# Performance work log

Hardware: AMD Instinct MI355X
Metric: run time of the kernel (lower is better)

The kernel has to match this reference:

```python
import jax, jax.numpy as jnp
import numpy as np

LN_EPS = 1e-5


def layer_norm(x, gamma, beta):
    mu = jnp.mean(x, axis=-1, keepdims=True)
    var = jnp.mean(jnp.square(x - mu), axis=-1, keepdims=True)
    return (x - mu) * jax.lax.rsqrt(var + LN_EPS) * gamma + beta


def setup_inputs() -> dict:
    key = jax.random.key(0)
    ks = jax.random.split(key, 4)
    b, t, d, h, r = 4, 2048, 1024, 4096, 32
    x = jax.random.normal(ks[0], (b, t, d), dtype=jnp.float32)
    L = jax.random.normal(ks[1], (d, r), dtype=jnp.float32) * (1.0 / np.sqrt(d))
    W1 = jax.random.normal(ks[2], (d, h), dtype=jnp.float32) * (1.0 / np.sqrt(d))
    W2 = jax.random.normal(ks[3], (h, d), dtype=jnp.float32) * (1.0 / np.sqrt(h))
    return {
        "x": x, "L": L,
        "W1": W1, "b1": jnp.zeros((h,), jnp.float32),
        "W2": W2, "b2": jnp.zeros((d,), jnp.float32),
        "gamma1": jnp.ones((d,), jnp.float32), "beta1": jnp.zeros((d,), jnp.float32),
        "gamma2": jnp.ones((d,), jnp.float32), "beta2": jnp.zeros((d,), jnp.float32),
    }


def reference(x, L, W1, b1, W2, b2, gamma1, beta1, gamma2, beta2):
    d = x.shape[-1]
    # --- GeodesicAttention on norm1(x) ---
    hn = layer_norm(x, gamma1, beta1)  # (b,t,d)
    g = jnp.eye(d, dtype=x.dtype) + L @ L.T  # PSD metric G = I + L L^T, (d,d)
    # dist_sq[b,i,j] = (x_i - x_j)^T G (x_i - x_j)
    #               = q_i + q_j - 2 x_i^T G x_j   (quadratic expansion; avoids (b,t,t,d) diff tensor)
    xg = jnp.einsum('btd,de->bte', hn, g)          # G x, (b,t,d)
    q = jnp.einsum('btd,btd->bt', xg, hn)          # diag quadratic form, (b,t)
    cross = jnp.einsum('bid,bjd->bij', xg, hn)     # x_i^T G x_j, (b,t,t)
    dist_sq = q[:, :, None] + q[:, None, :] - 2.0 * cross
    attn = jax.nn.softmax(-dist_sq, axis=-1)       # (b,t,t)
    x = x + jnp.einsum('bij,bjd->bid', attn, hn)
    # --- MLP on norm2(x) ---
    hm = layer_norm(x, gamma2, beta2)
    hid = jax.nn.gelu(hm @ W1 + b1, approximate=False)
    x = x + hid @ W2 + b2
    return x
```

## Files before the change

kernel.cpp:

```cpp
#include <hip/hip_runtime.h>
#include <cstdint>

typedef float f32x4 __attribute__((ext_vector_type(4)));
typedef __bf16 bf16x8 __attribute__((ext_vector_type(8)));

#define AS1 __attribute__((address_space(1)))
#define AS3 __attribute__((address_space(3)))

__device__ __forceinline__ void gld_lds16(const void* g, void* l) {
    __builtin_amdgcn_global_load_lds((const AS1 void*)g, (AS3 void*)l, 16, 0, 0);
}

__device__ __forceinline__ unsigned short f2bf(float f) {
    unsigned u = __builtin_bit_cast(unsigned, f);
    u = u + 0x7fffu + ((u >> 16) & 1u);
    return (unsigned short)(u >> 16);
}
__device__ __forceinline__ float bf2f(unsigned short h) {
    unsigned u = ((unsigned)h) << 16;
    return __builtin_bit_cast(float, u);
}

__device__ __forceinline__ void bar() {
    asm volatile("" ::: "memory");
    __builtin_amdgcn_s_barrier();
    asm volatile("" ::: "memory");
}

template<int BN, int MODE>
__global__ __launch_bounds__(512, 2) void gemm_nt2(
    const unsigned short* __restrict__ A, long lda, long sAb,
    const unsigned short* __restrict__ B, long ldb, long sBb,
    void* C, long ldc, long sCb,
    const float* add, long ldadd, long sAddb,
    const float* __restrict__ bias, int K)
{
    constexpr int NR  = BN / 64;
    constexpr int BUF = 16384 + BN * 64;
    __shared__ char sm[4 * BUF];
    const int tid = threadIdx.x, lane = tid & 63, wid = tid >> 6;
    const int wr = wid >> 2, wc = wid & 3;

    const long zb = blockIdx.z;
    const int nwg  = gridDim.x * gridDim.y;
    const int orig = blockIdx.y * gridDim.x + blockIdx.x;
    const int q8 = nwg >> 3, r8 = nwg & 7;
    const int xcd = orig & 7;
    const int wg  = (xcd < r8 ? xcd * (q8 + 1) : r8 * (q8 + 1) + (xcd - r8) * q8) + (orig >> 3);
    const int bx = wg % gridDim.x, by = wg / gridDim.x;

    const char* Ab = (const char*)(A + zb * sAb + (long)by * 256 * lda);
    const char* Bb = (const char*)(B + zb * sBb + (long)bx * BN * ldb);
    const long ldaB = lda * 2, ldbB = ldb * 2;
    const int  grow = tid >> 2;
    const long gcol = (long)(tid & 3) * 16;

    auto stage = [&](int kt, int bi) {
        const char* As = Ab + (long)kt * 64 + gcol;
        const char* Bs = Bb + (long)kt * 64 + gcol;
        char* d = sm + bi * BUF + wid * 1024;
#pragma unroll
        for (int i = 0; i < 2; ++i)
            gld_lds16(As + (long)(i * 128 + grow) * ldaB, d + i * 8192);
#pragma unroll
        for (int i = 0; i < BN / 128; ++i)
            gld_lds16(Bs + (long)(i * 128 + grow) * ldbB, d + 16384 + i * 8192);
    };

    f32x4 acc[8][NR] = {};
    const int NT = K / 32;
    stage(0, 0);
    if (NT > 1) stage(1, 1);
    if (NT > 2) stage(2, 2);

    for (int t = 0; t < NT; ++t) {
        const int rem = NT - t;
        if (rem > 3) {
            stage(t + 3, (t + 3) & 3);
            if constexpr (BN == 256) asm volatile("s_waitcnt vmcnt(12)" ::: "memory");
            else                     asm volatile("s_waitcnt vmcnt(9)"  ::: "memory");
        } else if (rem == 3) {
            if constexpr (BN == 256) asm volatile("s_waitcnt vmcnt(8)" ::: "memory");
            else                     asm volatile("s_waitcnt vmcnt(6)" ::: "memory");
        } else if (rem == 2) {
            if constexpr (BN == 256) asm volatile("s_waitcnt vmcnt(4)" ::: "memory");
            else                     asm volatile("s_waitcnt vmcnt(3)" ::: "memory");
        } else {
            asm volatile("s_waitcnt vmcnt(0)" ::: "memory");
        }
        bar();

        const char* bufA = sm + (t & 3) * BUF;
        const char* bufB = bufA + 16384;
        bf16x8 af[8], bfr[NR];
#pragma unroll
        for (int m = 0; m < 8; ++m)
            af[m] = *(const bf16x8*)(bufA + (wr * 128 + m * 16 + (lane & 15)) * 64 + (lane >> 4) * 16);
#pragma unroll
        for (int n = 0; n < NR; ++n)
            bfr[n] = *(const bf16x8*)(bufB + (wc * 16 * NR + n * 16 + (lane & 15)) * 64 + (lane >> 4) * 16);
        __builtin_amdgcn_s_setprio(1);
#pragma unroll
        for (int m = 0; m < 8; ++m)
#pragma unroll
            for (int n = 0; n < NR; ++n)
                acc[m][n] = __builtin_amdgcn_mfma_f32_16x16x32_bf16(af[m], bfr[n], acc[m][n], 0, 0, 0);
        __builtin_amdgcn_s_setprio(0);
        asm volatile("s_waitcnt lgkmcnt(0)" ::: "memory");
        __builtin_amdgcn_sched_barrier(0);
        bar();
    }

    const long row0 = (long)by * 256 + wr * 128 + (lane >> 4) * 4;
    const long col0 = (long)bx * BN + wc * 16 * NR + (lane & 15);
#pragma unroll
    for (int m = 0; m < 8; ++m)
#pragma unroll
        for (int n = 0; n < NR; ++n)
#pragma unroll
            for (int j = 0; j < 4; ++j) {
                const long r = row0 + m * 16 + j;
                const long c = col0 + n * 16;
                const float v = acc[m][n][j];
                if (MODE == 0) {
                    ((float*)C)[zb * sCb + r * ldc + c] = v;
                } else if (MODE == 1) {
                    ((float*)C)[zb * sCb + r * ldc + c] = v + add[zb * sAddb + r * ldadd + c];
                } else if (MODE == 2) {
                    float tt = v + bias[c];
                    float gl = 0.5f * tt * (1.0f + erff(tt * 0.70710678118654752f));
                    ((unsigned short*)C)[zb * sCb + r * ldc + c] = f2bf(gl);
                } else {
                    ((float*)C)[zb * sCb + r * ldc + c] = v + bias[c] + add[zb * sAddb + r * ldadd + c];
                }
            }
}

__global__ __launch_bounds__(256) void ln_kernel(
    const float* __restrict__ x, const float* __restrict__ gamma, const float* __restrict__ beta,
    unsigned short* __restrict__ out, int ldout, float* qout, int pad)
{
    const int tid = threadIdx.x;
    const long row = blockIdx.x;
    float4 v = ((const float4*)(x + row * 1024))[tid];
    float s = v.x + v.y + v.z + v.w;
    float s2 = v.x * v.x + v.y * v.y + v.z * v.z + v.w * v.w;
#pragma unroll
    for (int off = 32; off; off >>= 1) {
        s  += __shfl_down(s, off);
        s2 += __shfl_down(s2, off);
    }
    __shared__ float red[12];
    const int lane = tid & 63, wid = tid >> 6;
    if (lane == 0) { red[wid] = s; red[4 + wid] = s2; }
    __syncthreads();
    s  = red[0] + red[1] + red[2] + red[3];
    s2 = red[4] + red[5] + red[6] + red[7];
    const float mu = s * (1.0f / 1024.0f);
    const float var = s2 * (1.0f / 1024.0f) - mu * mu;
    const float rs = rsqrtf(var + 1e-5f);
    const float4 g = ((const float4*)gamma)[tid];
    const float4 b = ((const float4*)beta)[tid];
    unsigned short o0 = f2bf((v.x - mu) * rs * g.x + b.x);
    unsigned short o1 = f2bf((v.y - mu) * rs * g.y + b.y);
    unsigned short o2 = f2bf((v.z - mu) * rs * g.z + b.z);
    unsigned short o3 = f2bf((v.w - mu) * rs * g.w + b.w);
    ushort4 ov; ov.x = o0; ov.y = o1; ov.z = o2; ov.w = o3;
    ((ushort4*)(out + row * (long)ldout))[tid] = ov;
    if (pad && tid < 32) out[row * (long)ldout + 1056 + tid] = 0;
    if (qout) {
        float y0 = bf2f(o0), y1 = bf2f(o1), y2 = bf2f(o2), y3 = bf2f(o3);
        float sq = y0 * y0 + y1 * y1 + y2 * y2 + y3 * y3;
#pragma unroll
        for (int off = 32; off; off >>= 1) sq += __shfl_down(sq, off);
        if (lane == 0) red[8 + wid] = sq;
        __syncthreads();
        if (tid == 0) qout[row] = red[8] + red[9] + red[10] + red[11];
    }
}

__global__ __launch_bounds__(256) void u_kernel(
    unsigned short* __restrict__ z, const float* __restrict__ L, float* __restrict__ q)
{
    const int tid = threadIdx.x;
    const long row = blockIdx.x;
    __shared__ float hn[1024];
    __shared__ float part[8][32];
    ushort4 uv = ((const ushort4*)(z + row * 1088))[tid];
    hn[tid * 4 + 0] = bf2f(uv.x);
    hn[tid * 4 + 1] = bf2f(uv.y);
    hn[tid * 4 + 2] = bf2f(uv.z);
    hn[tid * 4 + 3] = bf2f(uv.w);
    __syncthreads();
    const int j = tid & 31, grp = tid >> 5;
    float acc = 0.f;
    const float* Lp = L + j;
#pragma unroll 4
    for (int d = grp * 128; d < grp * 128 + 128; ++d)
        acc += hn[d] * Lp[(long)d * 32];
    part[grp][j] = acc;
    __syncthreads();
    if (tid < 32) {
        float u = 0.f;
#pragma unroll
        for (int g2 = 0; g2 < 8; ++g2) u += part[g2][tid];
        unsigned short ub = f2bf(u);
        z[row * 1088 + 1024 + tid] = ub;
        float uf = bf2f(ub);
        part[0][tid] = uf * uf;
    }
    __syncthreads();
    if (tid == 0) {
        float sq = 0.f;
#pragma unroll
        for (int t2 = 0; t2 < 32; ++t2) sq += part[0][t2];
        q[row] += sq;
    }
}

__global__ __launch_bounds__(256) void softmax_kernel(
    float* S, const float* qb)
{
    const int tid = threadIdx.x;
    const long i = blockIdx.x, bl = blockIdx.y;
    float* Sr = S + (bl * 2048 + i) * 2048;
    const float* qr = qb + bl * 2048;
    float l[8];
    float mx = -1e30f;
#pragma unroll
    for (int c2 = 0; c2 < 8; ++c2) {
        const int jj = tid + c2 * 256;
        l[c2] = 2.0f * Sr[jj] - qr[jj];
        mx = fmaxf(mx, l[c2]);
    }
#pragma unroll
    for (int off = 32; off; off >>= 1) mx = fmaxf(mx, __shfl_xor(mx, off));
    __shared__ float red[8];
    const int lane = tid & 63, wid = tid >> 6;
    if (lane == 0) red[wid] = mx;
    __syncthreads();
    mx = fmaxf(fmaxf(red[0], red[1]), fmaxf(red[2], red[3]));
    float sum = 0.f;
#pragma unroll
    for (int c2 = 0; c2 < 8; ++c2) { l[c2] = __expf(l[c2] - mx); sum += l[c2]; }
#pragma unroll
    for (int off = 32; off; off >>= 1) sum += __shfl_xor(sum, off);
    if (lane == 0) red[4 + wid] = sum;
    __syncthreads();
    sum = red[4] + red[5] + red[6] + red[7];
    const float inv = 1.0f / sum;
    unsigned short* Pr = (unsigned short*)S + (bl * 2048 + i) * 4096;
#pragma unroll
    for (int c2 = 0; c2 < 8; ++c2)
        Pr[tid + c2 * 256] = f2bf(l[c2] * inv);
}

__global__ __launch_bounds__(256) void transpose_v_kernel(
    const unsigned short* __restrict__ z, unsigned short* __restrict__ Vt, long sVtb)
{
    __shared__ unsigned short t[32][33];
    const int tid = threadIdx.x;
    const int tx = tid & 31, ty = tid >> 5;
    const long b = blockIdx.z;
    const long k0 = (long)blockIdx.x * 32, n0 = (long)blockIdx.y * 32;
#pragma unroll
    for (int r = 0; r < 32; r += 8)
        t[r + ty][tx] = z[(b * 2048 + k0 + r + ty) * 1088 + n0 + tx];
    __syncthreads();
#pragma unroll
    for (int r = 0; r < 32; r += 8)
        Vt[b * sVtb + (n0 + r + ty) * 2048 + k0 + tx] = t[tx][r + ty];
}

__global__ __launch_bounds__(256) void cast_transpose_kernel(
    const float* __restrict__ W, unsigned short* __restrict__ Wt, int rows, int cols)
{
    __shared__ float t[32][33];
    const int tid = threadIdx.x;
    const int tx = tid & 31, ty = tid >> 5;
    const long r0 = (long)blockIdx.y * 32, c0 = (long)blockIdx.x * 32;
#pragma unroll
    for (int r = 0; r < 32; r += 8)
        t[r + ty][tx] = W[(r0 + r + ty) * (long)cols + c0 + tx];
    __syncthreads();
#pragma unroll
    for (int r = 0; r < 32; r += 8)
        Wt[(c0 + r + ty) * (long)rows + r0 + tx] = f2bf(t[tx][r + ty]);
}

extern "C" void kernel_launch(void* const* d_in, const int* in_sizes, int n_in,
                              void* d_out, int out_size, void* d_ws, size_t ws_size,
                              hipStream_t stream)
{
    const float* x   = (const float*)d_in[0];
    const float* L   = (const float*)d_in[1];
    const float* W1  = (const float*)d_in[2];
    const float* b1  = (const float*)d_in[3];
    const float* W2  = (const float*)d_in[4];
    const float* b2  = (const float*)d_in[5];
    const float* g1  = (const float*)d_in[6];
    const float* be1 = (const float*)d_in[7];
    const float* g2  = (const float*)d_in[8];
    const float* be2 = (const float*)d_in[9];
    float* out = (float*)d_out;
    unsigned short* z = (unsigned short*)d_out;

    char* wsp = (char*)d_ws;
    float* q = (float*)wsp;
    char* pool = wsp + 32768;
    unsigned short* Vt   = (unsigned short*)pool;
    float*          Smat = (float*)(pool + 16777216);
    unsigned short* W1t = (unsigned short*)pool;
    unsigned short* W2t = (unsigned short*)(pool + 8388608);
    unsigned short* hm  = (unsigned short*)(pool + 16777216);
    unsigned short* hid = (unsigned short*)(pool + 33554432);
    const bool fullMLP = ws_size >= (size_t)32768 + 100663296 + 65536;

    ln_kernel<<<8192, 256, 0, stream>>>(x, g1, be1, z, 1088, q, 1);
    u_kernel<<<8192, 256, 0, stream>>>(z, L, q);

    transpose_v_kernel<<<dim3(64, 32, 4), 256, 0, stream>>>(z, Vt, (long)1024 * 2048);
    gemm_nt2<256, 0><<<dim3(8, 8, 4), 512, 0, stream>>>(
        z, 1088, (long)2048 * 1088,
        z, 1088, (long)2048 * 1088,
        Smat, 2048, (long)2048 * 2048,
        nullptr, 0, 0, nullptr, 1088);
    softmax_kernel<<<dim3(2048, 4), 256, 0, stream>>>(Smat, q);
    gemm_nt2<128, 1><<<dim3(8, 8, 4), 512, 0, stream>>>(
        (const unsigned short*)Smat, 4096, (long)2048 * 4096,
        Vt, 2048, (long)1024 * 2048,
        out, 1024, (long)2048 * 1024,
        x, 1024, (long)2048 * 1024,
        nullptr, 2048);

    cast_transpose_kernel<<<dim3(128, 32), 256, 0, stream>>>(W1, W1t, 1024, 4096);
    cast_transpose_kernel<<<dim3(32, 128), 256, 0, stream>>>(W2, W2t, 4096, 1024);
    ln_kernel<<<8192, 256, 0, stream>>>(out, g2, be2, hm, 1024, nullptr, 0);
    if (fullMLP) {
        gemm_nt2<256, 2><<<dim3(16, 32, 1), 512, 0, stream>>>(
            hm, 1024, 0, W1t, 1024, 0,
            hid, 4096, 0, nullptr, 0, 0, b1, 1024);
        gemm_nt2<128, 3><<<dim3(8, 32, 1), 512, 0, stream>>>(
            hid, 4096, 0, W2t, 4096, 0,
            out, 1024, 0, out, 1024, 0, b2, 4096);
    } else {
        for (int c = 0; c < 2; ++c) {
            const unsigned short* hmc = hm + (size_t)c * 4096 * 1024;
            float* oc = out + (size_t)c * 4096 * 1024;
            gemm_nt2<256, 2><<<dim3(16, 16, 1), 512, 0, stream>>>(
                hmc, 1024, 0, W1t, 1024, 0,
                hid, 4096, 0, nullptr, 0, 0, b1, 1024);
            gemm_nt2<128, 3><<<dim3(8, 16, 1), 512, 0, stream>>>(
                hid, 4096, 0, W2t, 4096, 0,
                oc, 1024, 0, oc, 1024, 0, b2, 4096);
        }
    }
}
```

Before: 392.8 us.

## Swizzle LDS tile layout and double-buffer MFMA fragments across k-steps

Each lane's 16-byte global column chunk is now chosen by an XOR swizzle, and the fragment reads use the matching swizzled offset. This spreads LDS reads across banks to cut bank conflicts. The main loop is also unrolled by two with two register sets of A/B fragments, so the next tile's LDS reads are issued before the current tile's MFMAs and overlap with them. The cost is more register pressure from the doubled fragment arrays. The loop also assumes the k-tile count is even, which holds for all call sites here.

Result: faster. 381.7 us (-2.8%).

```diff
diff --git a/kernel.cpp b/kernel.cpp
--- a/kernel.cpp
+++ b/kernel.cpp
@@ -27,8 +27,12 @@
     asm volatile("" ::: "memory");
 }
 
+#define WAITVM(n) asm volatile("s_waitcnt vmcnt(" #n ")" ::: "memory")
+#define LGKM0     asm volatile("s_waitcnt lgkmcnt(0)" ::: "memory")
+#define SCHED0    __builtin_amdgcn_sched_barrier(0)
+
 template<int BN, int MODE>
-__global__ __launch_bounds__(512, 2) void gemm_nt2(
+__global__ __launch_bounds__(512, 2) void gemm_nt3(
     const unsigned short* __restrict__ A, long lda, long sAb,
     const unsigned short* __restrict__ B, long ldb, long sBb,
     void* C, long ldc, long sCb,
@@ -53,11 +57,12 @@
     const char* Bb = (const char*)(B + zb * sBb + (long)bx * BN * ldb);
     const long ldaB = lda * 2, ldbB = ldb * 2;
     const int  grow = tid >> 2;
-    const long gcol = (long)(tid & 3) * 16;
+    const long gsw  = (long)((((lane & 3) ^ ((lane >> 2) & 3) ^ ((lane >> 4) & 1))) << 4);
+    const int  koff16 = (((lane >> 4) ^ (lane & 3) ^ ((lane >> 2) & 1)) << 4);
 
     auto stage = [&](int kt, int bi) {
-        const char* As = Ab + (long)kt * 64 + gcol;
-        const char* Bs = Bb + (long)kt * 64 + gcol;
+        const char* As = Ab + (long)kt * 64 + gsw;
+        const char* Bs = Bb + (long)kt * 64 + gsw;
         char* d = sm + bi * BUF + wid * 1024;
 #pragma unroll
         for (int i = 0; i < 2; ++i)
@@ -67,38 +72,18 @@
             gld_lds16(Bs + (long)(i * 128 + grow) * ldbB, d + 16384 + i * 8192);
     };
 
+    auto rdfrags = [&](const char* bufA, bf16x8* af, bf16x8* bfr) {
+        const char* bufB = bufA + 16384;
+#pragma unroll
+        for (int m = 0; m < 8; ++m)
+            af[m] = *(const bf16x8*)(bufA + (wr * 128 + m * 16 + (lane & 15)) * 64 + koff16);
+#pragma unroll
+        for (int n = 0; n < NR; ++n)
+            bfr[n] = *(const bf16x8*)(bufB + (wc * 16 * NR + n * 16 + (lane & 15)) * 64 + koff16);
+    };
+
     f32x4 acc[8][NR] = {};
-    const int NT = K / 32;
-    stage(0, 0);
-    if (NT > 1) stage(1, 1);
-    if (NT > 2) stage(2, 2);
-
-    for (int t = 0; t < NT; ++t) {
-        const int rem = NT - t;
-        if (rem > 3) {
-            stage(t + 3, (t + 3) & 3);
-            if constexpr (BN == 256) asm volatile("s_waitcnt vmcnt(12)" ::: "memory");
-            else                     asm volatile("s_waitcnt vmcnt(9)"  ::: "memory");
-        } else if (rem == 3) {
-            if constexpr (BN == 256) asm volatile("s_waitcnt vmcnt(8)" ::: "memory");
-            else                     asm volatile("s_waitcnt vmcnt(6)" ::: "memory");
-        } else if (rem == 2) {
-            if constexpr (BN == 256) asm volatile("s_waitcnt vmcnt(4)" ::: "memory");
-            else                     asm volatile("s_waitcnt vmcnt(3)" ::: "memory");
-        } else {
-            asm volatile("s_waitcnt vmcnt(0)" ::: "memory");
-        }
-        bar();
-
-        const char* bufA = sm + (t & 3) * BUF;
-        const char* bufB = bufA + 16384;
-        bf16x8 af[8], bfr[NR];
-#pragma unroll
-        for (int m = 0; m < 8; ++m)
-            af[m] = *(const bf16x8*)(bufA + (wr * 128 + m * 16 + (lane & 15)) * 64 + (lane >> 4) * 16);
-#pragma unroll
-        for (int n = 0; n < NR; ++n)
-            bfr[n] = *(const bf16x8*)(bufB + (wc * 16 * NR + n * 16 + (lane & 15)) * 64 + (lane >> 4) * 16);
+    auto domfma = [&](const bf16x8* af, const bf16x8* bfr) {
         __builtin_amdgcn_s_setprio(1);
 #pragma unroll
         for (int m = 0; m < 8; ++m)
@@ -106,9 +91,44 @@
             for (int n = 0; n < NR; ++n)
                 acc[m][n] = __builtin_amdgcn_mfma_f32_16x16x32_bf16(af[m], bfr[n], acc[m][n], 0, 0, 0);
         __builtin_amdgcn_s_setprio(0);
-        asm volatile("s_waitcnt lgkmcnt(0)" ::: "memory");
-        __builtin_amdgcn_sched_barrier(0);
+    };
+
+    const int NT = K / 32;
+    bf16x8 a0[8], b0[NR], a1[8], b1[NR];
+
+    stage(0, 0); stage(1, 1); stage(2, 2);
+    if constexpr (BN == 256) WAITVM(8); else WAITVM(6);
+    bar();
+    rdfrags(sm, a0, b0);
+    SCHED0;
+
+#pragma unroll 1
+    for (int t = 0; t < NT; t += 2) {
+        if (t + 3 < NT) {
+            stage(t + 3, (t + 3) & 3);
+            if constexpr (BN == 256) WAITVM(8); else WAITVM(6);
+        } else {
+            WAITVM(0);
+        }
         bar();
+        rdfrags(sm + ((t + 1) & 3) * BUF, a1, b1);
+        SCHED0;
+        domfma(a0, b0);
+        LGKM0; SCHED0;
+
+        if (t + 2 < NT) {
+            if (t + 4 < NT) {
+                stage(t + 4, (t + 4) & 3);
+                if constexpr (BN == 256) WAITVM(8); else WAITVM(6);
+            } else {
+                if constexpr (BN == 256) WAITVM(4); else WAITVM(3);
+            }
+            bar();
+            rdfrags(sm + ((t + 2) & 3) * BUF, a0, b0);
+            SCHED0;
+        }
+        domfma(a1, b1);
+        LGKM0; SCHED0;
     }
 
     const long row0 = (long)by * 256 + wr * 128 + (lane >> 4) * 4;
@@ -320,13 +340,13 @@
     u_kernel<<<8192, 256, 0, stream>>>(z, L, q);
 
     transpose_v_kernel<<<dim3(64, 32, 4), 256, 0, stream>>>(z, Vt, (long)1024 * 2048);
-    gemm_nt2<256, 0><<<dim3(8, 8, 4), 512, 0, stream>>>(
+    gemm_nt3<256, 0><<<dim3(8, 8, 4), 512, 0, stream>>>(
         z, 1088, (long)2048 * 1088,
         z, 1088, (long)2048 * 1088,
         Smat, 2048, (long)2048 * 2048,
         nullptr, 0, 0, nullptr, 1088);
     softmax_kernel<<<dim3(2048, 4), 256, 0, stream>>>(Smat, q);
-    gemm_nt2<128, 1><<<dim3(8, 8, 4), 512, 0, stream>>>(
+    gemm_nt3<128, 1><<<dim3(8, 8, 4), 512, 0, stream>>>(
         (const unsigned short*)Smat, 4096, (long)2048 * 4096,
         Vt, 2048, (long)1024 * 2048,
         out, 1024, (long)2048 * 1024,
@@ -337,20 +357,20 @@
     cast_transpose_kernel<<<dim3(32, 128), 256, 0, stream>>>(W2, W2t, 4096, 1024);
     ln_kernel<<<8192, 256, 0, stream>>>(out, g2, be2, hm, 1024, nullptr, 0);
     if (fullMLP) {
-        gemm_nt2<256, 2><<<dim3(16, 32, 1), 512, 0, stream>>>(
+        gemm_nt3<256, 2><<<dim3(16, 32, 1), 512, 0, stream>>>(
             hm, 1024, 0, W1t, 1024, 0,
             hid, 4096, 0, nullptr, 0, 0, b1, 1024);
-        gemm_nt2<128, 3><<<dim3(8, 32, 1), 512, 0, stream>>>(
+        gemm_nt3<128, 3><<<dim3(8, 32, 1), 512, 0, stream>>>(
             hid, 4096, 0, W2t, 4096, 0,
             out, 1024, 0, out, 1024, 0, b2, 4096);
     } else {
         for (int c = 0; c < 2; ++c) {
             const unsigned short* hmc = hm + (size_t)c * 4096 * 1024;
             float* oc = out + (size_t)c * 4096 * 1024;
-            gemm_nt2<256, 2><<<dim3(16, 16, 1), 512, 0, stream>>>(
+            gemm_nt3<256, 2><<<dim3(16, 16, 1), 512, 0, stream>>>(
                 hmc, 1024, 0, W1t, 1024, 0,
                 hid, 4096, 0, nullptr, 0, 0, b1, 1024);
-            gemm_nt2<128, 3><<<dim3(8, 16, 1), 512, 0, stream>>>(
+            gemm_nt3<128, 3><<<dim3(8, 16, 1), 512, 0, stream>>>(
                 hid, 4096, 0, W2t, 4096, 0,
                 oc, 1024, 0, oc, 1024, 0, b2, 4096);
         }
```

## Restructure GEMM into double-buffered 8-phase pipeline with swizzled LDS and K=64 tiles

Applied to the files above, without the earlier changes.

Replaces the 4-deep K=32 pipelined GEMM with a 2-buffer K=64 scheme. Each K tile is split into four phases that interleave half-tile global-to-LDS loads with MFMA work, and each phase has its own barrier and waitcnt. An XOR swizzle is applied to the LDS layout to avoid bank conflicts on fragment reads. The goal is finer-grained overlap of loads and compute and less LDS conflict, at the cost of more barriers and tighter vmcnt bookkeeping, which could go wrong for edge K counts. K=1088 gives NT=17, which is fine.

Result: no change. 389.5 us (-0.9%).

```diff
diff --git a/kernel.cpp b/kernel.cpp
--- a/kernel.cpp
+++ b/kernel.cpp
@@ -27,17 +27,23 @@
     asm volatile("" ::: "memory");
 }
 
+#define WAITVM(n) asm volatile("s_waitcnt vmcnt(" #n ")" ::: "memory")
+#define LGKM0     asm volatile("s_waitcnt lgkmcnt(0)" ::: "memory")
+#define SCHED0    __builtin_amdgcn_sched_barrier(0)
+
 template<int BN, int MODE>
-__global__ __launch_bounds__(512, 2) void gemm_nt2(
+__global__ __launch_bounds__(512, 2) void gemm8p(
     const unsigned short* __restrict__ A, long lda, long sAb,
     const unsigned short* __restrict__ B, long ldb, long sBb,
     void* C, long ldc, long sCb,
     const float* add, long ldadd, long sAddb,
     const float* __restrict__ bias, int K)
 {
-    constexpr int NR  = BN / 64;
-    constexpr int BUF = 16384 + BN * 64;
-    __shared__ char sm[4 * BUF];
+    constexpr int NR   = BN / 64;
+    constexpr int ABUF = 256 * 128;
+    constexpr int BBUF = BN * 128;
+    constexpr int BUF  = ABUF + BBUF;
+    __shared__ char sm[2 * BUF];
     const int tid = threadIdx.x, lane = tid & 63, wid = tid >> 6;
     const int wr = wid >> 2, wc = wid & 3;
 
@@ -52,64 +58,73 @@
     const char* Ab = (const char*)(A + zb * sAb + (long)by * 256 * lda);
     const char* Bb = (const char*)(B + zb * sBb + (long)bx * BN * ldb);
     const long ldaB = lda * 2, ldbB = ldb * 2;
-    const int  grow = tid >> 2;
-    const long gcol = (long)(tid & 3) * 16;
-
-    auto stage = [&](int kt, int bi) {
-        const char* As = Ab + (long)kt * 64 + gcol;
-        const char* Bs = Bb + (long)kt * 64 + gcol;
-        char* d = sm + bi * BUF + wid * 1024;
-#pragma unroll
-        for (int i = 0; i < 2; ++i)
-            gld_lds16(As + (long)(i * 128 + grow) * ldaB, d + i * 8192);
-#pragma unroll
-        for (int i = 0; i < BN / 128; ++i)
-            gld_lds16(Bs + (long)(i * 128 + grow) * ldbB, d + 16384 + i * 8192);
+
+    auto stageA = [&](int kt, int p, int half) {
+#pragma unroll
+        for (int i = 0; i < 2; ++i) {
+            const int r0 = half * 64 + i * 128;
+            const int r  = r0 + (tid >> 3);
+            gld_lds16(Ab + (long)r * ldaB + (long)kt * 128 + (((tid & 7) ^ (r & 7)) << 4),
+                      sm + p * BUF + r0 * 128 + wid * 1024);
+        }
     };
+    auto stageB = [&](int kt, int p, int ks) {
+#pragma unroll
+        for (int i = 0; i < BN / 128; ++i) {
+            const int r = i * 128 + (tid >> 2);
+            gld_lds16(Bb + (long)r * ldbB + (long)kt * 128 + ks * 64 + (((tid & 3) ^ ((r >> 1) & 3)) << 4),
+                      sm + p * BUF + ABUF + ks * BN * 64 + i * 8192 + wid * 1024);
+        }
+    };
 
     f32x4 acc[8][NR] = {};
-    const int NT = K / 32;
-    stage(0, 0);
-    if (NT > 1) stage(1, 1);
-    if (NT > 2) stage(2, 2);
-
+    const int NT = K / 64;
+
+#define PHASE(MH, KS, STAGE_STMT) do {                                          \
+    bf16x8 af[4]; bf16x8 bfr[NR];                                               \
+    _Pragma("unroll")                                                           \
+    for (int m = 0; m < 4; ++m) {                                               \
+        const int R = wr * 128 + ((MH) * 4 + m) * 16 + (lane & 15);             \
+        const int cc = (((KS) * 4 + (lane >> 4)) ^ (R & 7)) << 4;               \
+        af[m] = *(const bf16x8*)(bufp + R * 128 + cc);                          \
+    }                                                                           \
+    _Pragma("unroll")                                                           \
+    for (int n = 0; n < NR; ++n) {                                              \
+        const int R = wc * 16 * NR + n * 16 + (lane & 15);                      \
+        const int cc = ((lane >> 4) ^ ((R >> 1) & 3)) << 4;                     \
+        bfr[n] = *(const bf16x8*)(bufp + ABUF + (KS) * BN * 64 + R * 64 + cc);  \
+    }                                                                           \
+    STAGE_STMT;                                                                 \
+    if (t < NT - 2) { if constexpr (BN == 256) WAITVM(8); else WAITVM(6); }     \
+    else WAITVM(0);                                                             \
+    bar();                                                                      \
+    LGKM0; SCHED0;                                                              \
+    __builtin_amdgcn_s_setprio(1);                                              \
+    _Pragma("unroll")                                                           \
+    for (int m = 0; m < 4; ++m)                                                 \
+    _Pragma("unroll")                                                           \
+        for (int n = 0; n < NR; ++n)                                            \
+            acc[(MH) * 4 + m][n] = __builtin_amdgcn_mfma_f32_16x16x32_bf16(     \
+                af[m], bfr[n], acc[(MH) * 4 + m][n], 0, 0, 0);                  \
+    __builtin_amdgcn_s_setprio(0);                                              \
+    bar();                                                                      \
+} while (0)
+
+    stageA(0, 0, 0); stageA(0, 0, 1); stageB(0, 0, 0); stageB(0, 0, 1);
+    stageA(1, 1, 0); stageB(1, 1, 0); stageA(1, 1, 1); stageB(1, 1, 1);
+    if constexpr (BN == 256) WAITVM(8); else WAITVM(6);
+    bar();
+
+#pragma unroll 1
     for (int t = 0; t < NT; ++t) {
-        const int rem = NT - t;
-        if (rem > 3) {
-            stage(t + 3, (t + 3) & 3);
-            if constexpr (BN == 256) asm volatile("s_waitcnt vmcnt(12)" ::: "memory");
-            else                     asm volatile("s_waitcnt vmcnt(9)"  ::: "memory");
-        } else if (rem == 3) {
-            if constexpr (BN == 256) asm volatile("s_waitcnt vmcnt(8)" ::: "memory");
-            else                     asm volatile("s_waitcnt vmcnt(6)" ::: "memory");
-        } else if (rem == 2) {
-            if constexpr (BN == 256) asm volatile("s_waitcnt vmcnt(4)" ::: "memory");
-            else                     asm volatile("s_waitcnt vmcnt(3)" ::: "memory");
-        } else {
-            asm volatile("s_waitcnt vmcnt(0)" ::: "memory");
-        }
-        bar();
-
-        const char* bufA = sm + (t & 3) * BUF;
-        const char* bufB = bufA + 16384;
-        bf16x8 af[8], bfr[NR];
-#pragma unroll
-        for (int m = 0; m < 8; ++m)
-            af[m] = *(const bf16x8*)(bufA + (wr * 128 + m * 16 + (lane & 15)) * 64 + (lane >> 4) * 16);
-#pragma unroll
-        for (int n = 0; n < NR; ++n)
-            bfr[n] = *(const bf16x8*)(bufB + (wc * 16 * NR + n * 16 + (lane & 15)) * 64 + (lane >> 4) * 16);
-        __builtin_amdgcn_s_setprio(1);
-#pragma unroll
-        for (int m = 0; m < 8; ++m)
-#pragma unroll
-            for (int n = 0; n < NR; ++n)
-                acc[m][n] = __builtin_amdgcn_mfma_f32_16x16x32_bf16(af[m], bfr[n], acc[m][n], 0, 0, 0);
-        __builtin_amdgcn_s_setprio(0);
-        asm volatile("s_waitcnt lgkmcnt(0)" ::: "memory");
-        __builtin_amdgcn_sched_barrier(0);
-        bar();
-    }
+        const int p = t & 1;
+        const char* bufp = sm + p * BUF;
+        PHASE(0, 0, { if (t >= 1 && t + 1 < NT) stageA(t + 1, p ^ 1, 1); });
+        PHASE(1, 0, { if (t >= 1 && t + 1 < NT) stageB(t + 1, p ^ 1, 1); });
+        PHASE(0, 1, { if (t + 2 < NT) stageB(t + 2, p, 0); });
+        PHASE(1, 1, { if (t + 2 < NT) stageA(t + 2, p, 0); });
+    }
+#undef PHASE
 
     const long row0 = (long)by * 256 + wr * 128 + (lane >> 4) * 4;
     const long col0 = (long)bx * BN + wc * 16 * NR + (lane & 15);
@@ -320,13 +335,13 @@
     u_kernel<<<8192, 256, 0, stream>>>(z, L, q);
 
     transpose_v_kernel<<<dim3(64, 32, 4), 256, 0, stream>>>(z, Vt, (long)1024 * 2048);
-    gemm_nt2<256, 0><<<dim3(8, 8, 4), 512, 0, stream>>>(
+    gemm8p<256, 0><<<dim3(8, 8, 4), 512, 0, stream>>>(
         z, 1088, (long)2048 * 1088,
         z, 1088, (long)2048 * 1088,
         Smat, 2048, (long)2048 * 2048,
         nullptr, 0, 0, nullptr, 1088);
     softmax_kernel<<<dim3(2048, 4), 256, 0, stream>>>(Smat, q);
-    gemm_nt2<128, 1><<<dim3(8, 8, 4), 512, 0, stream>>>(
+    gemm8p<128, 1><<<dim3(8, 8, 4), 512, 0, stream>>>(
         (const unsigned short*)Smat, 4096, (long)2048 * 4096,
         Vt, 2048, (long)1024 * 2048,
         out, 1024, (long)2048 * 1024,
@@ -337,20 +352,20 @@
     cast_transpose_kernel<<<dim3(32, 128), 256, 0, stream>>>(W2, W2t, 4096, 1024);
     ln_kernel<<<8192, 256, 0, stream>>>(out, g2, be2, hm, 1024, nullptr, 0);
     if (fullMLP) {
-        gemm_nt2<256, 2><<<dim3(16, 32, 1), 512, 0, stream>>>(
+        gemm8p<256, 2><<<dim3(16, 32, 1), 512, 0, stream>>>(
             hm, 1024, 0, W1t, 1024, 0,
             hid, 4096, 0, nullptr, 0, 0, b1, 1024);
-        gemm_nt2<128, 3><<<dim3(8, 32, 1), 512, 0, stream>>>(
+        gemm8p<128, 3><<<dim3(8, 32, 1), 512, 0, stream>>>(
             hid, 4096, 0, W2t, 4096, 0,
             out, 1024, 0, out, 1024, 0, b2, 4096);
     } else {
         for (int c = 0; c < 2; ++c) {
             const unsigned short* hmc = hm + (size_t)c * 4096 * 1024;
             float* oc = out + (size_t)c * 4096 * 1024;
-            gemm_nt2<256, 2><<<dim3(16, 16, 1), 512, 0, stream>>>(
+            gemm8p<256, 2><<<dim3(16, 16, 1), 512, 0, stream>>>(
                 hmc, 1024, 0, W1t, 1024, 0,
                 hid, 4096, 0, nullptr, 0, 0, b1, 1024);
-            gemm_nt2<128, 3><<<dim3(8, 16, 1), 512, 0, stream>>>(
+            gemm8p<128, 3><<<dim3(8, 16, 1), 512, 0, stream>>>(
                 hid, 4096, 0, W2t, 4096, 0,
                 oc, 1024, 0, oc, 1024, 0, b2, 4096);
         }
```
